# Optimization experiments

Hardware: AMD Instinct MI355X
Metric: run time of the kernel (lower is better)

Reference implementation:

```python
import jax, jax.numpy as jnp
import numpy as np


def setup_inputs() -> dict:
    key = jax.random.key(0)
    x = jax.random.uniform(key, (64_000_000,), dtype=jnp.float32)
    return {"x": x, "bins": 100}


def reference(x, bins):
    # torch.histc semantics with min=max=0.0: use data min/max as the range.
    xf = x.reshape(-1)
    hmin = jnp.min(xf)
    hmax = jnp.max(xf)
    # guard degenerate range (torch widens it; with random data this is a no-op)
    hmax = jnp.where(hmax == hmin, hmin + 1.0, hmax)
    scale = bins / (hmax - hmin)
    # bin index: floor((x - min) * bins / (max - min)); value == max lands in last bin
    idx = jnp.clip(jnp.floor((xf - hmin) * scale).astype(jnp.int32), 0, bins - 1)
    in_range = (xf >= hmin) & (xf <= hmax)  # out-of-range elements are ignored
    weights = in_range.astype(xf.dtype)
    hist = jax.ops.segment_sum(weights, idx, num_segments=bins)
    return hist
```

## Files before the change

### kernel.cpp

```cpp
#include <hip/hip_runtime.h>

#define NBLOCKS   1024
#define NTHREADS  256
#define WPB       (NTHREADS / 64)
#define UNROLL_A  8
#define UNROLL_B  8
#define NCOPIES   64
#define CSTRIDE   101

#define WS_PMIN   0
#define WS_PMAX   NBLOCKS
#define WS_META   (2 * NBLOCKS)
#define WS_BHIST  (2 * NBLOCKS + 64)

__device__ unsigned g_gmin = 0;
__device__ unsigned g_gmax = 0;

__global__ __launch_bounds__(NTHREADS, 4)
void histc_pass1(const float4* __restrict__ x4, long n4,
                 const float* __restrict__ xtail, long ntail,
                 float* __restrict__ ws, float* __restrict__ out, int bins) {
    __shared__ unsigned sh[NCOPIES * CSTRIDE];
    __shared__ float sred[2 * WPB];

    const int lane = threadIdx.x & 63;
    const int wid  = threadIdx.x >> 6;

    const unsigned gb0 = g_gmin, gb1 = g_gmax;
    const float ghmin  = __uint_as_float(gb0);
    const float gscale = (float)bins / (__uint_as_float(gb1) - ghmin);

    for (int b = threadIdx.x; b < NCOPIES * CSTRIDE; b += blockDim.x) sh[b] = 0u;
    if (blockIdx.x == 0) {
        for (int b = threadIdx.x; b < bins; b += blockDim.x) out[b] = 0.0f;
        if (threadIdx.x == 0) {
            ((unsigned*)ws)[WS_META]     = gb0;
            ((unsigned*)ws)[WS_META + 1] = gb1;
        }
    }
    __syncthreads();

    const long gwave  = blockIdx.x * (long)WPB + wid;
    const long nwaves = (long)gridDim.x * WPB;
    const int  bmax   = bins - 1;
    unsigned*  h      = sh + lane * CSTRIDE;

    float m0 = INFINITY, M0 = -INFINITY, m1 = INFINITY, M1 = -INFINITY;

    const long SEG  = 64 * UNROLL_A;
    const long nseg = n4 / SEG;

    {
        const long tid = blockIdx.x * (long)blockDim.x + threadIdx.x;
        const long nth = (long)gridDim.x * blockDim.x;
        for (long j = nseg * SEG + tid; j < n4; j += nth) {
            float4 v = x4[j];
            m0 = fminf(m0, fminf(v.x, v.y)); m1 = fminf(m1, fminf(v.z, v.w));
            M0 = fmaxf(M0, fmaxf(v.x, v.y)); M1 = fmaxf(M1, fmaxf(v.z, v.w));
            int b0 = max(0, min((int)((v.x - ghmin) * gscale), bmax));
            int b1 = max(0, min((int)((v.y - ghmin) * gscale), bmax));
            int b2 = max(0, min((int)((v.z - ghmin) * gscale), bmax));
            int b3 = max(0, min((int)((v.w - ghmin) * gscale), bmax));
            atomicAdd(&h[b0], 1u); atomicAdd(&h[b1], 1u);
            atomicAdd(&h[b2], 1u); atomicAdd(&h[b3], 1u);
        }
        for (long j = tid; j < ntail; j += nth) {
            float v = xtail[j];
            m0 = fminf(m0, v); M0 = fmaxf(M0, v);
            int b0 = max(0, min((int)((v - ghmin) * gscale), bmax));
            atomicAdd(&h[b0], 1u);
        }
    }

    for (long s = nseg - 1 - gwave; s >= 0; s -= nwaves) {
        const float4* p = x4 + s * SEG + lane;
        float4 v[UNROLL_A];
        #pragma unroll
        for (int u = 0; u < UNROLL_A; ++u) v[u] = p[u * 64];
        #pragma unroll
        for (int u = 0; u < UNROLL_A; ++u) {
            m0 = fminf(m0, fminf(v[u].x, v[u].y));
            m1 = fminf(m1, fminf(v[u].z, v[u].w));
            M0 = fmaxf(M0, fmaxf(v[u].x, v[u].y));
            M1 = fmaxf(M1, fmaxf(v[u].z, v[u].w));
            int b0 = max(0, min((int)((v[u].x - ghmin) * gscale), bmax));
            int b1 = max(0, min((int)((v[u].y - ghmin) * gscale), bmax));
            int b2 = max(0, min((int)((v[u].z - ghmin) * gscale), bmax));
            int b3 = max(0, min((int)((v[u].w - ghmin) * gscale), bmax));
            atomicAdd(&h[b0], 1u); atomicAdd(&h[b1], 1u);
            atomicAdd(&h[b2], 1u); atomicAdd(&h[b3], 1u);
        }
    }

    float lm = fminf(m0, m1), lM = fmaxf(M0, M1);
    for (int off = 32; off; off >>= 1) {
        lm = fminf(lm, __shfl_xor(lm, off));
        lM = fmaxf(lM, __shfl_xor(lM, off));
    }
    if (lane == 0) { sred[wid] = lm; sred[WPB + wid] = lM; }
    __syncthreads();
    if (threadIdx.x == 0) {
        float bm = sred[0], bM = sred[WPB];
        for (int w = 1; w < WPB; ++w) { bm = fminf(bm, sred[w]); bM = fmaxf(bM, sred[WPB + w]); }
        ws[WS_PMIN + blockIdx.x] = bm;
        ws[WS_PMAX + blockIdx.x] = bM;
    }

    for (int b = threadIdx.x; b < bins; b += blockDim.x) {
        unsigned t = 0;
        #pragma unroll 8
        for (int c = 0; c < NCOPIES; ++c) t += sh[c * CSTRIDE + b];
        ws[WS_BHIST + (long)blockIdx.x * bins + b] = (float)t;
    }
}

__global__ __launch_bounds__(NTHREADS, 4)
void histc_pass2(const float4* __restrict__ x4, long n4,
                 const float* __restrict__ xtail, long ntail,
                 float* __restrict__ ws, float* __restrict__ out, int bins) {
    __shared__ unsigned sh[NCOPIES * CSTRIDE];
    __shared__ float sred[2 * WPB];
    __shared__ float srange[2];
    __shared__ unsigned svalid;

    const int lane = threadIdx.x & 63;
    const int wid  = threadIdx.x >> 6;

    float rm = INFINITY, rM = -INFINITY;
    for (int i = threadIdx.x; i < NBLOCKS; i += blockDim.x) {
        rm = fminf(rm, ws[WS_PMIN + i]);
        rM = fmaxf(rM, ws[WS_PMAX + i]);
    }
    for (int off = 32; off; off >>= 1) {
        rm = fminf(rm, __shfl_xor(rm, off));
        rM = fmaxf(rM, __shfl_xor(rM, off));
    }
    if (lane == 0) { sred[wid] = rm; sred[WPB + wid] = rM; }
    __syncthreads();
    if (threadIdx.x == 0) {
        float bm = sred[0], bM = sred[WPB];
        for (int w = 1; w < WPB; ++w) { bm = fminf(bm, sred[w]); bM = fmaxf(bM, sred[WPB + w]); }
        if (bM == bm) bM = bm + 1.0f;
        unsigned tb0 = __float_as_uint(bm), tb1 = __float_as_uint(bM);
        unsigned u0 = ((unsigned*)ws)[WS_META], u1 = ((unsigned*)ws)[WS_META + 1];
        svalid = (tb0 == u0 && tb1 == u1 && u0 != u1) ? 1u : 0u;
        srange[0] = bm;
        srange[1] = (float)bins / (bM - bm);
        if (blockIdx.x == 0) { g_gmin = tb0; g_gmax = tb1; }
    }
    __syncthreads();

    if (svalid) {
        const int b = blockIdx.x;
        if (b < bins) {
            float t = 0.0f;
            for (int k = threadIdx.x; k < NBLOCKS; k += blockDim.x)
                t += ws[WS_BHIST + (long)k * bins + b];
            for (int off = 32; off; off >>= 1) t += __shfl_xor(t, off);
            if (lane == 0) sred[wid] = t;
            __syncthreads();
            if (threadIdx.x == 0) {
                float s = sred[0];
                for (int w = 1; w < WPB; ++w) s += sred[w];
                out[b] = s;
            }
        }
        return;
    }

    for (int b = threadIdx.x; b < NCOPIES * CSTRIDE; b += blockDim.x) sh[b] = 0u;
    __syncthreads();

    const float hmin  = srange[0];
    const float scale = srange[1];
    const int   bmax  = bins - 1;
    unsigned*   h     = sh + lane * CSTRIDE;

    const long gwave  = blockIdx.x * (long)WPB + wid;
    const long nwaves = (long)gridDim.x * WPB;
    const long SEG    = 64 * UNROLL_B;
    const long nseg   = n4 / SEG;

    for (long s = gwave; s < nseg; s += nwaves) {
        const float4* p = x4 + s * SEG + lane;
        float4 v[UNROLL_B];
        #pragma unroll
        for (int u = 0; u < UNROLL_B; ++u) v[u] = p[u * 64];
        #pragma unroll
        for (int u = 0; u < UNROLL_B; ++u) {
            int b0 = min((int)((v[u].x - hmin) * scale), bmax);
            int b1 = min((int)((v[u].y - hmin) * scale), bmax);
            int b2 = min((int)((v[u].z - hmin) * scale), bmax);
            int b3 = min((int)((v[u].w - hmin) * scale), bmax);
            atomicAdd(&h[b0], 1u); atomicAdd(&h[b1], 1u);
            atomicAdd(&h[b2], 1u); atomicAdd(&h[b3], 1u);
        }
    }
    {
        const long tid = blockIdx.x * (long)blockDim.x + threadIdx.x;
        const long nth = (long)gridDim.x * blockDim.x;
        for (long j = nseg * SEG + tid; j < n4; j += nth) {
            float4 v = x4[j];
            int b0 = min((int)((v.x - hmin) * scale), bmax);
            int b1 = min((int)((v.y - hmin) * scale), bmax);
            int b2 = min((int)((v.z - hmin) * scale), bmax);
            int b3 = min((int)((v.w - hmin) * scale), bmax);
            atomicAdd(&h[b0], 1u); atomicAdd(&h[b1], 1u);
            atomicAdd(&h[b2], 1u); atomicAdd(&h[b3], 1u);
        }
        for (long j = tid; j < ntail; j += nth) {
            int b0 = min((int)((xtail[j] - hmin) * scale), bmax);
            atomicAdd(&h[b0], 1u);
        }
    }
    __syncthreads();

    for (int b = threadIdx.x; b < bins; b += blockDim.x) {
        unsigned t = 0;
        #pragma unroll 8
        for (int c = 0; c < NCOPIES; ++c) t += sh[c * CSTRIDE + b];
        if (t) atomicAdd(&out[b], (float)t);
    }
}

extern "C" void kernel_launch(void* const* d_in, const int* in_sizes, int n_in,
                              void* d_out, int out_size, void* d_ws, size_t ws_size,
                              hipStream_t stream) {
    const float* x = (const float*)d_in[0];
    long n = (long)in_sizes[0];
    int bins = out_size;

    long n4 = n >> 2;
    long ntail = n - (n4 << 2);
    const float4* x4 = (const float4*)x;
    const float* xtail = x + (n4 << 2);

    float* out = (float*)d_out;
    float* ws  = (float*)d_ws;

    histc_pass1<<<NBLOCKS, NTHREADS, 0, stream>>>(x4, n4, xtail, ntail, ws, out, bins);
    histc_pass2<<<NBLOCKS, NTHREADS, 0, stream>>>(x4, n4, xtail, ntail, ws, out, bins);
}
```

Before: 347.6 us.

## Double-buffer segment loads in pass1 and simplify bin clamping

Restructures the main streaming loop of pass1 into a two-buffer software pipeline. The next segment's eight float4 loads are issued before the current segment's min/max and LDS atomic work, and sched_barrier keeps the compiler from reordering across that point, so memory latency can overlap with compute. Bin index clamping also switches to a single unsigned min instead of max/min. The second buffer doubles the registers held per thread, which may pressure occupancy under launch_bounds(256,4).

```diff
diff --git a/kernel.cpp b/kernel.cpp
--- a/kernel.cpp
+++ b/kernel.cpp
@@ -16,6 +16,11 @@
 __device__ unsigned g_gmin = 0;
 __device__ unsigned g_gmax = 0;
 
+static __device__ __forceinline__ int bidx(float x, float h, float s, int bmax) {
+    unsigned b = (unsigned)(int)((x - h) * s);
+    return (int)min(b, (unsigned)bmax);
+}
+
 __global__ __launch_bounds__(NTHREADS, 4)
 void histc_pass1(const float4* __restrict__ x4, long n4,
                  const float* __restrict__ xtail, long ntail,
@@ -57,42 +62,69 @@
             float4 v = x4[j];
             m0 = fminf(m0, fminf(v.x, v.y)); m1 = fminf(m1, fminf(v.z, v.w));
             M0 = fmaxf(M0, fmaxf(v.x, v.y)); M1 = fmaxf(M1, fmaxf(v.z, v.w));
-            int b0 = max(0, min((int)((v.x - ghmin) * gscale), bmax));
-            int b1 = max(0, min((int)((v.y - ghmin) * gscale), bmax));
-            int b2 = max(0, min((int)((v.z - ghmin) * gscale), bmax));
-            int b3 = max(0, min((int)((v.w - ghmin) * gscale), bmax));
-            atomicAdd(&h[b0], 1u); atomicAdd(&h[b1], 1u);
-            atomicAdd(&h[b2], 1u); atomicAdd(&h[b3], 1u);
+            atomicAdd(&h[bidx(v.x, ghmin, gscale, bmax)], 1u);
+            atomicAdd(&h[bidx(v.y, ghmin, gscale, bmax)], 1u);
+            atomicAdd(&h[bidx(v.z, ghmin, gscale, bmax)], 1u);
+            atomicAdd(&h[bidx(v.w, ghmin, gscale, bmax)], 1u);
         }
         for (long j = tid; j < ntail; j += nth) {
             float v = xtail[j];
             m0 = fminf(m0, v); M0 = fmaxf(M0, v);
-            int b0 = max(0, min((int)((v - ghmin) * gscale), bmax));
-            atomicAdd(&h[b0], 1u);
-        }
-    }
-
-    for (long s = nseg - 1 - gwave; s >= 0; s -= nwaves) {
-        const float4* p = x4 + s * SEG + lane;
-        float4 v[UNROLL_A];
-        #pragma unroll
-        for (int u = 0; u < UNROLL_A; ++u) v[u] = p[u * 64];
-        #pragma unroll
-        for (int u = 0; u < UNROLL_A; ++u) {
-            m0 = fminf(m0, fminf(v[u].x, v[u].y));
-            m1 = fminf(m1, fminf(v[u].z, v[u].w));
-            M0 = fmaxf(M0, fmaxf(v[u].x, v[u].y));
-            M1 = fmaxf(M1, fmaxf(v[u].z, v[u].w));
-            int b0 = max(0, min((int)((v[u].x - ghmin) * gscale), bmax));
-            int b1 = max(0, min((int)((v[u].y - ghmin) * gscale), bmax));
-            int b2 = max(0, min((int)((v[u].z - ghmin) * gscale), bmax));
-            int b3 = max(0, min((int)((v[u].w - ghmin) * gscale), bmax));
-            atomicAdd(&h[b0], 1u); atomicAdd(&h[b1], 1u);
-            atomicAdd(&h[b2], 1u); atomicAdd(&h[b3], 1u);
-        }
-    }
-
-    float lm = fminf(m0, m1), lM = fmaxf(M0, M1);
+            atomicAdd(&h[bidx(v, ghmin, gscale, bmax)], 1u);
+        }
+    }
+
+#define LOAD8(dst, sidx)                                                     \
+    {                                                                        \
+        const float4* p_ = x4 + (sidx) * SEG + lane;                         \
+        _Pragma("unroll")                                                    \
+        for (int u_ = 0; u_ < UNROLL_A; ++u_) dst[u_] = p_[u_ * 64];         \
+    }
+
+#define COMP8(src)                                                           \
+    {                                                                        \
+        _Pragma("unroll")                                                    \
+        for (int u_ = 0; u_ < UNROLL_A; ++u_) {                              \
+            float4 v_ = src[u_];                                             \
+            m0 = fminf(m0, fminf(v_.x, v_.y));                               \
+            m1 = fminf(m1, fminf(v_.z, v_.w));                               \
+            M0 = fmaxf(M0, fmaxf(v_.x, v_.y));                               \
+            M1 = fmaxf(M1, fmaxf(v_.z, v_.w));                               \
+            atomicAdd(&h[bidx(v_.x, ghmin, gscale, bmax)], 1u);              \
+            atomicAdd(&h[bidx(v_.y, ghmin, gscale, bmax)], 1u);              \
+            atomicAdd(&h[bidx(v_.z, ghmin, gscale, bmax)], 1u);              \
+            atomicAdd(&h[bidx(v_.w, ghmin, gscale, bmax)], 1u);              \
+        }                                                                    \
+    }
+
+    {
+        float4 va[UNROLL_A], vb[UNROLL_A];
+        long sa = nseg - 1 - gwave;
+        if (sa >= 0) LOAD8(va, sa);
+        long sb = sa - nwaves;
+        while (sb >= 0) {
+            LOAD8(vb, sb);
+            __builtin_amdgcn_sched_barrier(0);
+            COMP8(va);
+            sa = sb - nwaves;
+            if (sa >= 0) {
+                LOAD8(va, sa);
+                __builtin_amdgcn_sched_barrier(0);
+                COMP8(vb);
+                sb = sa - nwaves;
+            } else {
+                COMP8(vb);
+                sa = -1;
+                break;
+            }
+        }
+        if (sa >= 0) COMP8(va);
+    }
+#undef LOAD8
+#undef COMP8
+
+    float lm = fminf(m0, m1);
+    float lM = fmaxf(M0, M1);
     for (int off = 32; off; off >>= 1) {
         lm = fminf(lm, __shfl_xor(lm, off));
         lM = fmaxf(lM, __shfl_xor(lM, off));
```

Measured after the change: 347.4 us. No clear change (-0.1%).
